# Kernel tuning notes

Measured on AMD Instinct MI355X. Metric: run time of the kernel, lower is better.

The kernel has to match this reference:

```python
import jax, jax.numpy as jnp
import numpy as np

B, L, D = 8, 2048, 1024
H = 16            # n_heads
E = 8             # num_experts
TOPK = 2
DH = D // H       # 64, per-head dim (== expert Linear dim)
CAP = TOPK * L // E  # 512 tokens per expert per batch (exact by construction)


def setup_inputs() -> dict:
    key = jax.random.key(0)
    ks = jax.random.split(key, 6)
    x = jax.random.normal(ks[0], (B, L, D), dtype=jnp.float32)
    gating_output = jax.nn.softmax(
        jax.random.normal(ks[1], (B, L, E), dtype=jnp.float32), axis=-1)
    # deterministic balanced routing: token l -> experts (l%E, (l+E//2)%E)
    l = jnp.arange(L)
    ind = jnp.stack([l % E, (l + E // 2) % E], axis=-1)  # [L,2]
    indices = jnp.broadcast_to(ind[None], (B, L, TOPK)).astype(jnp.int64)
    s = 1.0 / np.sqrt(DH)
    W1 = jax.random.normal(ks[2], (DH, DH), dtype=jnp.float32) * s
    b1 = jax.random.normal(ks[3], (DH,), dtype=jnp.float32) * 0.01
    W2 = jax.random.normal(ks[4], (DH, DH), dtype=jnp.float32) * s
    b2 = jax.random.normal(ks[5], (DH,), dtype=jnp.float32) * 0.01
    return {"x": x, "gating_output": gating_output, "indices": indices,
            "W1": W1, "b1": b1, "W2": W2, "b2": b2}


def _expert(xh, W1, b1, W2, b2):
    # xh: [B,H,C,d]. Shared expert (expert_fix) applied to gathered tokens.
    q = jnp.einsum('bhcd,ed->bhce', xh, W1) + b1
    k = jnp.einsum('bhcd,ed->bhce', xh, W2) + b2
    adj = jax.nn.gelu(jnp.einsum('bhid,bhjd->bhij', q, k), approximate=False)
    adj = jax.nn.softmax(adj, axis=-1)  # dropout: identity in eval
    out = jnp.einsum('bhij,bhjd->bhid', adj, xh)
    Bb, Hh, C, d = out.shape
    return out.transpose(0, 2, 1, 3).reshape(Bb, C, Hh * d)  # [B,C,D]


def reference(x, gating_output, indices, W1, b1, W2, b2):
    Bx, Lx, Dx = x.shape
    final = jnp.zeros_like(x)
    brow = jnp.arange(Bx)[:, None]  # [B,1]
    for i in range(E):
        mask = (indices == i).any(axis=-1)  # [B,L] bool, exactly CAP true/row
        idx = jax.vmap(lambda m: jnp.nonzero(m, size=CAP)[0])(mask)  # [B,C]
        xt = jnp.take_along_axis(x, idx[:, :, None], axis=1)  # [B,C,D]
        xh = xt.reshape(Bx, CAP, H, DH).transpose(0, 2, 1, 3)  # [B,H,C,d]
        out = _expert(xh, W1, b1, W2, b2)  # [B,C,D]
        g = jnp.take_along_axis(gating_output[..., i], idx, axis=1)  # [B,C]
        final = final.at[brow, idx].add(out * g[:, :, None])
    return final
```

## Files before the change

### kernel.cpp

```cpp
#include <hip/hip_runtime.h>
#include <hip/hip_bf16.h>
#include <cmath>


typedef _Float16 h16;
typedef __attribute__((ext_vector_type(4))) _Float16 half4;
typedef __attribute__((ext_vector_type(8))) _Float16 half8;
typedef __attribute__((ext_vector_type(4))) float f32x4;
typedef __attribute__((ext_vector_type(4))) unsigned int uint4v;

#define B_ 8
#define L_ 2048
#define D_ 1024
#define H_ 16
#define DH_ 64
#define L2E 1.4426950408f

#define XT_LD 520
#define XT_OFF 0
#define KW_OFF 66560
#define BETA_OFF 132096
#define AUX_OFF 134144
#define WC_OFF 134672
#define SMEM_BYTES 143888

__device__ __forceinline__ float gelu_fast(float v) {
  float e = __builtin_amdgcn_exp2f(v * fmaf(v * v, -0.10294357f, -2.3021957f));
  return v * __builtin_amdgcn_rcpf(1.f + e);
}

__global__ __launch_bounds__(512) void moe_prewc(
    const float* __restrict__ W1, const float* __restrict__ b1,
    const float* __restrict__ W2, const float* __restrict__ b2,
    float* __restrict__ ws)
{
  int bx = blockIdx.x;
  if (bx < 8) {
    int t = bx * 512 + threadIdx.x;
    int d = t >> 6, f = t & 63;
    float acc = 0.f;
    for (int e = 0; e < 64; ++e) acc += W2[e * 64 + f] * W1[e * 64 + d];
    ws[t] = acc;
  } else {
    int tid = threadIdx.x;
    if (tid < 64) {
      float acc = 0.f;
      for (int e = 0; e < 64; ++e) acc += b2[e] * W1[e * 64 + tid];
      ws[4096 + tid] = acc;
    } else if (tid < 128) {
      int f = tid - 64; float acc = 0.f;
      for (int e = 0; e < 64; ++e) acc += b1[e] * W2[e * 64 + f];
      ws[4160 + f] = acc;
    } else if (tid == 128) {
      float acc = 0.f;
      for (int e = 0; e < 64; ++e) acc += b1[e] * b2[e];
      ws[4224] = acc;
    }
  }
}

__global__ __launch_bounds__(1024) void moe_attn(
    const float* __restrict__ x, const float* __restrict__ gating,
    const float* __restrict__ wsc, float* __restrict__ out)
{
  extern __shared__ char smem[];
  h16*   XTh  = (h16*)(smem + XT_OFF);
  char*  KWb  = smem + KW_OFF;
  float* beta = (float*)(smem + BETA_OFF);
  float* bc   = (float*)(smem + AUX_OFF);
  float* wb   = bc + 64;
  float* bbp  = wb + 64;
  h16*   WCh  = (h16*)(smem + WC_OFF);

  const int tid  = threadIdx.x;
  const int wave = tid >> 6;
  const int lane = tid & 63;
  const int l15  = lane & 15;
  const int lg   = lane >> 4;
  const int bx   = blockIdx.x;
  const int h    = bx & 15;
  const int m    = (bx >> 4) & 3;
  const int b    = bx >> 6;

  for (int t = tid; t < 4096; t += 1024) {
    int c = t >> 3, dc = t & 7;
    int l = 8 * (c >> 1) + m + 4 * (c & 1);
    const float* gp = x + ((size_t)(b * L_ + l)) * D_ + h * DH_ + dc * 8;
    float vv[8];
    *(float4*)(vv)     = *(const float4*)(gp);
    *(float4*)(vv + 4) = *(const float4*)(gp + 4);
#pragma unroll
    for (int j = 0; j < 8; ++j)
      XTh[(dc * 8 + j) * XT_LD + c] = (h16)vv[j];
  }
  for (int t = tid; t < 4096; t += 1024)
    WCh[(t >> 6) * 72 + (t & 63)] = (h16)wsc[t];
  if (tid < 64) bc[tid] = wsc[4096 + tid];
  else if (tid < 128) wb[tid - 64] = wsc[4096 + tid];
  else if (tid == 128) *bbp = wsc[4224];
  __syncthreads();

  if (tid < 512) {
    int n = tid;
    float acc = *bbp;
    for (int f = 0; f < 64; ++f) acc += (float)XTh[f * XT_LD + n] * wb[f];
    beta[n] = acc;
  }
  for (int mt = wave; mt < 32; mt += 16) {
    int n0 = mt * 16;
    int tok = n0 + l15;
    half8 a0, a1;
#pragma unroll
    for (int j = 0; j < 8; ++j) {
      a0[j] = XTh[(lg * 8 + j) * XT_LD + tok];
      a1[j] = XTh[(32 + lg * 8 + j) * XT_LD + tok];
    }
#pragma unroll
    for (int ct = 0; ct < 4; ++ct) {
      const half8 bw0 = *(const half8*)(WCh + (ct * 16 + l15) * 72 + lg * 8);
      const half8 bw1 = *(const half8*)(WCh + (ct * 16 + l15) * 72 + 32 + lg * 8);
      f32x4 acc = {0.f, 0.f, 0.f, 0.f};
      acc = __builtin_amdgcn_mfma_f32_16x16x32_f16(a0, bw0, acc, 0, 0, 0);
      acc = __builtin_amdgcn_mfma_f32_16x16x32_f16(a1, bw1, acc, 0, 0, 0);
      int d = ct * 16 + l15;
      float bcd = bc[d];
#pragma unroll
      for (int r = 0; r < 4; ++r) {
        int row = n0 + lg * 4 + r;
        int byteoff = row * 128 + ((((d >> 3) ^ (row & 7)) << 4) | ((d & 7) << 1));
        *(h16*)(KWb + byteoff) = (h16)(acc[r] + bcd);
      }
    }
  }
  __syncthreads();

  const int g0 = (lg ^ (l15 & 7)) << 4;
  const int g1 = ((4 + lg) ^ (l15 & 7)) << 4;

  for (int qi = 0; qi < 2; ++qi) {
    const int m0 = (wave + qi * 16) * 16;
    const int qrow = m0 + l15;
    const int ql = 8 * (qrow >> 1) + m + 4 * (qrow & 1);
    const float* qp = x + ((size_t)(b * L_ + ql)) * D_ + h * DH_;

    half8 bq0, bq1;
    {
      const float4 A0 = *(const float4*)(qp + lg * 8);
      const float4 A1 = *(const float4*)(qp + lg * 8 + 4);
      const float4 B0 = *(const float4*)(qp + 32 + lg * 8);
      const float4 B1 = *(const float4*)(qp + 32 + lg * 8 + 4);
      bq0[0] = (h16)A0.x; bq0[1] = (h16)A0.y; bq0[2] = (h16)A0.z; bq0[3] = (h16)A0.w;
      bq0[4] = (h16)A1.x; bq0[5] = (h16)A1.y; bq0[6] = (h16)A1.z; bq0[7] = (h16)A1.w;
      bq1[0] = (h16)B0.x; bq1[1] = (h16)B0.y; bq1[2] = (h16)B0.z; bq1[3] = (h16)B0.w;
      bq1[4] = (h16)B1.x; bq1[5] = (h16)B1.y; bq1[6] = (h16)B1.z; bq1[7] = (h16)B1.w;
    }

    f32x4 o0 = {0.f,0.f,0.f,0.f}, o1 = o0, o2 = o0, o3 = o0;
    float Sl = 0.f, R = -1e30f, Ml2 = 0.f;

    for (int it = 0; it < 16; ++it) {
      f32x4 sa0, sa1;
      {
        int t = it * 2;
        f32x4 bv = *(const f32x4*)(beta + t * 16 + lg * 4);
        const char* kr = KWb + (t * 16 + l15) * 128;
        half8 ka0 = *(const half8*)(kr + g0);
        half8 ka1 = *(const half8*)(kr + g1);
        bv  = __builtin_amdgcn_mfma_f32_16x16x32_f16(ka0, bq0, bv, 0, 0, 0);
        sa0 = __builtin_amdgcn_mfma_f32_16x16x32_f16(ka1, bq1, bv, 0, 0, 0);
      }
      {
        int t = it * 2 + 1;
        f32x4 bv = *(const f32x4*)(beta + t * 16 + lg * 4);
        const char* kr = KWb + (t * 16 + l15) * 128;
        half8 ka0 = *(const half8*)(kr + g0);
        half8 ka1 = *(const half8*)(kr + g1);
        bv  = __builtin_amdgcn_mfma_f32_16x16x32_f16(ka0, bq0, bv, 0, 0, 0);
        sa1 = __builtin_amdgcn_mfma_f32_16x16x32_f16(ka1, bq1, bv, 0, 0, 0);
      }
      float cm = fmaxf(fmaxf(fmaxf(sa0[0], sa0[1]), fmaxf(sa0[2], sa0[3])),
                       fmaxf(fmaxf(sa1[0], sa1[1]), fmaxf(sa1[2], sa1[3])));
      cm = fmaxf(cm, __shfl_xor(cm, 16));
      cm = fmaxf(cm, __shfl_xor(cm, 32));
      bool tr = cm > R + 8.f;
      if (__any(tr)) {
        float Rn = tr ? cm : R;
        float Mn = fmaxf(gelu_fast(Rn), 0.f);
        float Ml2n = Mn * L2E;
        float scl = __builtin_amdgcn_exp2f(Ml2 - Ml2n);
        Sl *= scl; o0 *= scl; o1 *= scl; o2 *= scl; o3 *= scl;
        R = Rn; Ml2 = Ml2n;
      }
      float p00 = __builtin_amdgcn_exp2f(fmaf(gelu_fast(sa0[0]), L2E, -Ml2));
      float p01 = __builtin_amdgcn_exp2f(fmaf(gelu_fast(sa0[1]), L2E, -Ml2));
      float p02 = __builtin_amdgcn_exp2f(fmaf(gelu_fast(sa0[2]), L2E, -Ml2));
      float p03 = __builtin_amdgcn_exp2f(fmaf(gelu_fast(sa0[3]), L2E, -Ml2));
      float p10 = __builtin_amdgcn_exp2f(fmaf(gelu_fast(sa1[0]), L2E, -Ml2));
      float p11 = __builtin_amdgcn_exp2f(fmaf(gelu_fast(sa1[1]), L2E, -Ml2));
      float p12 = __builtin_amdgcn_exp2f(fmaf(gelu_fast(sa1[2]), L2E, -Ml2));
      float p13 = __builtin_amdgcn_exp2f(fmaf(gelu_fast(sa1[3]), L2E, -Ml2));
      Sl += ((p00 + p01) + (p02 + p03)) + ((p10 + p11) + (p12 + p13));
      uint4v pw;
      pw[0] = __builtin_bit_cast(unsigned int, __builtin_amdgcn_cvt_pkrtz(p00, p01));
      pw[1] = __builtin_bit_cast(unsigned int, __builtin_amdgcn_cvt_pkrtz(p02, p03));
      pw[2] = __builtin_bit_cast(unsigned int, __builtin_amdgcn_cvt_pkrtz(p10, p11));
      pw[3] = __builtin_bit_cast(unsigned int, __builtin_amdgcn_cvt_pkrtz(p12, p13));
      const half8 pB = __builtin_bit_cast(half8, pw);
      {
        const h16* ap = XTh + l15 * XT_LD + it * 32 + lg * 4;
#pragma unroll
        for (int ct = 0; ct < 4; ++ct) {
          const h16* app = ap + ct * 16 * XT_LD;
          const half4 lo = *(const half4*)(app);
          const half4 hi = *(const half4*)(app + 16);
          const half8 av = {lo[0], lo[1], lo[2], lo[3], hi[0], hi[1], hi[2], hi[3]};
          if      (ct == 0) o0 = __builtin_amdgcn_mfma_f32_16x16x32_f16(av, pB, o0, 0, 0, 0);
          else if (ct == 1) o1 = __builtin_amdgcn_mfma_f32_16x16x32_f16(av, pB, o1, 0, 0, 0);
          else if (ct == 2) o2 = __builtin_amdgcn_mfma_f32_16x16x32_f16(av, pB, o2, 0, 0, 0);
          else              o3 = __builtin_amdgcn_mfma_f32_16x16x32_f16(av, pB, o3, 0, 0, 0);
        }
      }
    }
    float Sv = Sl;
    Sv += __shfl_xor(Sv, 16);
    Sv += __shfl_xor(Sv, 32);
    const float* gp = gating + ((size_t)(b * L_ + ql)) * 8;
    float gv = gp[m] + gp[m + 4];
    float scale = gv * __builtin_amdgcn_rcpf(Sv);
    float* op = out + ((size_t)(b * L_ + ql)) * D_ + h * DH_ + lg * 4;
    *(f32x4*)(op)      = o0 * scale;
    *(f32x4*)(op + 16) = o1 * scale;
    *(f32x4*)(op + 32) = o2 * scale;
    *(f32x4*)(op + 48) = o3 * scale;
  }
}

extern "C" void kernel_launch(void* const* d_in, const int* in_sizes, int n_in,
                              void* d_out, int out_size, void* d_ws, size_t ws_size,
                              hipStream_t stream) {
  const float* x      = (const float*)d_in[0];
  const float* gating = (const float*)d_in[1];
  const float* W1 = (const float*)d_in[3];
  const float* b1 = (const float*)d_in[4];
  const float* W2 = (const float*)d_in[5];
  const float* b2 = (const float*)d_in[6];
  float* ws = (float*)d_ws;

  static bool attr_set = false;
  if (!attr_set) {
    hipFuncSetAttribute(reinterpret_cast<const void*>(moe_attn),
                        hipFuncAttributeMaxDynamicSharedMemorySize, SMEM_BYTES);
    attr_set = true;
  }
  moe_prewc<<<dim3(9), dim3(512), 0, stream>>>(W1, b1, W2, b2, ws);
  moe_attn<<<dim3(512), dim3(1024), SMEM_BYTES, stream>>>(
      x, gating, ws, (float*)d_out);
}
```

Before: 115.0 us.

## Process both query tiles per wave together to reuse K and X loads

The two sequential query-tile passes are fused into one loop, so each wave processes two 16-row query tiles at once. Each K fragment and X fragment read from shared memory then feeds two MFMAs. The XOR-swizzled K layout is replaced by a padded pitch of 136 bytes, and launch bounds now request waves-per-EU 4. The aim is to halve LDS traffic per MFMA and give the scheduler more independent MFMA work, at the cost of more registers for two accumulator sets and extra shared memory.

New measurement: 126.0 us. +9.6%, slower.

```diff
diff --git a/kernel.cpp b/kernel.cpp
--- a/kernel.cpp
+++ b/kernel.cpp
@@ -18,11 +18,12 @@
 
 #define XT_LD 520
 #define XT_OFF 0
+#define KW_PITCH 136
 #define KW_OFF 66560
-#define BETA_OFF 132096
-#define AUX_OFF 134144
-#define WC_OFF 134672
-#define SMEM_BYTES 143888
+#define BETA_OFF 136192
+#define AUX_OFF 138240
+#define WC_OFF 138768
+#define SMEM_BYTES 147984
 
 __device__ __forceinline__ float gelu_fast(float v) {
   float e = __builtin_amdgcn_exp2f(v * fmaf(v * v, -0.10294357f, -2.3021957f));
@@ -59,7 +60,7 @@
   }
 }
 
-__global__ __launch_bounds__(1024) void moe_attn(
+__global__ __launch_bounds__(1024, 4) void moe_attn(
     const float* __restrict__ x, const float* __restrict__ gating,
     const float* __restrict__ wsc, float* __restrict__ out)
 {
@@ -127,111 +128,181 @@
 #pragma unroll
       for (int r = 0; r < 4; ++r) {
         int row = n0 + lg * 4 + r;
-        int byteoff = row * 128 + ((((d >> 3) ^ (row & 7)) << 4) | ((d & 7) << 1));
-        *(h16*)(KWb + byteoff) = (h16)(acc[r] + bcd);
+        *(h16*)(KWb + row * KW_PITCH + d * 2) = (h16)(acc[r] + bcd);
       }
     }
   }
   __syncthreads();
 
-  const int g0 = (lg ^ (l15 & 7)) << 4;
-  const int g1 = ((4 + lg) ^ (l15 & 7)) << 4;
-
-  for (int qi = 0; qi < 2; ++qi) {
-    const int m0 = (wave + qi * 16) * 16;
-    const int qrow = m0 + l15;
-    const int ql = 8 * (qrow >> 1) + m + 4 * (qrow & 1);
-    const float* qp = x + ((size_t)(b * L_ + ql)) * D_ + h * DH_;
-
-    half8 bq0, bq1;
+  const int g0 = lg * 16;
+  const int g1 = 64 + lg * 16;
+
+  const int m0a = wave * 16;
+  const int m0b = (wave + 16) * 16;
+  const int qra = m0a + l15, qrb = m0b + l15;
+  const int qla = 8 * (qra >> 1) + m + 4 * (qra & 1);
+  const int qlb = 8 * (qrb >> 1) + m + 4 * (qrb & 1);
+  const float* qpa = x + ((size_t)(b * L_ + qla)) * D_ + h * DH_;
+  const float* qpb = x + ((size_t)(b * L_ + qlb)) * D_ + h * DH_;
+
+  half8 bqa0, bqa1, bqb0, bqb1;
+  {
+    const float4 A0 = *(const float4*)(qpa + lg * 8);
+    const float4 A1 = *(const float4*)(qpa + lg * 8 + 4);
+    const float4 A2 = *(const float4*)(qpa + 32 + lg * 8);
+    const float4 A3 = *(const float4*)(qpa + 32 + lg * 8 + 4);
+    bqa0[0]=(h16)A0.x; bqa0[1]=(h16)A0.y; bqa0[2]=(h16)A0.z; bqa0[3]=(h16)A0.w;
+    bqa0[4]=(h16)A1.x; bqa0[5]=(h16)A1.y; bqa0[6]=(h16)A1.z; bqa0[7]=(h16)A1.w;
+    bqa1[0]=(h16)A2.x; bqa1[1]=(h16)A2.y; bqa1[2]=(h16)A2.z; bqa1[3]=(h16)A2.w;
+    bqa1[4]=(h16)A3.x; bqa1[5]=(h16)A3.y; bqa1[6]=(h16)A3.z; bqa1[7]=(h16)A3.w;
+    const float4 B0 = *(const float4*)(qpb + lg * 8);
+    const float4 B1 = *(const float4*)(qpb + lg * 8 + 4);
+    const float4 B2 = *(const float4*)(qpb + 32 + lg * 8);
+    const float4 B3 = *(const float4*)(qpb + 32 + lg * 8 + 4);
+    bqb0[0]=(h16)B0.x; bqb0[1]=(h16)B0.y; bqb0[2]=(h16)B0.z; bqb0[3]=(h16)B0.w;
+    bqb0[4]=(h16)B1.x; bqb0[5]=(h16)B1.y; bqb0[6]=(h16)B1.z; bqb0[7]=(h16)B1.w;
+    bqb1[0]=(h16)B2.x; bqb1[1]=(h16)B2.y; bqb1[2]=(h16)B2.z; bqb1[3]=(h16)B2.w;
+    bqb1[4]=(h16)B3.x; bqb1[5]=(h16)B3.y; bqb1[6]=(h16)B3.z; bqb1[7]=(h16)B3.w;
+  }
+
+  f32x4 oa0 = {0.f,0.f,0.f,0.f}, oa1 = oa0, oa2 = oa0, oa3 = oa0;
+  f32x4 ob0 = oa0, ob1 = oa0, ob2 = oa0, ob3 = oa0;
+  float Sla = 0.f, Ra = -1e30f, Mla = 0.f;
+  float Slb = 0.f, Rb = -1e30f, Mlb = 0.f;
+
+  for (int it = 0; it < 16; ++it) {
+    const int t0 = it * 2, t1 = it * 2 + 1;
+    const char* kr0 = KWb + (t0 * 16 + l15) * KW_PITCH;
+    const char* kr1 = KWb + (t1 * 16 + l15) * KW_PITCH;
+    const half8 ka00 = *(const half8*)(kr0 + g0);
+    const half8 ka01 = *(const half8*)(kr0 + g1);
+    const half8 ka10 = *(const half8*)(kr1 + g0);
+    const half8 ka11 = *(const half8*)(kr1 + g1);
+    const f32x4 bv0 = *(const f32x4*)(beta + t0 * 16 + lg * 4);
+    const f32x4 bv1 = *(const f32x4*)(beta + t1 * 16 + lg * 4);
+
+    f32x4 s0a = __builtin_amdgcn_mfma_f32_16x16x32_f16(ka00, bqa0, bv0, 0, 0, 0);
+    s0a = __builtin_amdgcn_mfma_f32_16x16x32_f16(ka01, bqa1, s0a, 0, 0, 0);
+    f32x4 s1a = __builtin_amdgcn_mfma_f32_16x16x32_f16(ka10, bqa0, bv1, 0, 0, 0);
+    s1a = __builtin_amdgcn_mfma_f32_16x16x32_f16(ka11, bqa1, s1a, 0, 0, 0);
+    f32x4 s0b = __builtin_amdgcn_mfma_f32_16x16x32_f16(ka00, bqb0, bv0, 0, 0, 0);
+    s0b = __builtin_amdgcn_mfma_f32_16x16x32_f16(ka01, bqb1, s0b, 0, 0, 0);
+    f32x4 s1b = __builtin_amdgcn_mfma_f32_16x16x32_f16(ka10, bqb0, bv1, 0, 0, 0);
+    s1b = __builtin_amdgcn_mfma_f32_16x16x32_f16(ka11, bqb1, s1b, 0, 0, 0);
+
+    float cma = fmaxf(fmaxf(fmaxf(s0a[0], s0a[1]), fmaxf(s0a[2], s0a[3])),
+                      fmaxf(fmaxf(s1a[0], s1a[1]), fmaxf(s1a[2], s1a[3])));
+    float cmb = fmaxf(fmaxf(fmaxf(s0b[0], s0b[1]), fmaxf(s0b[2], s0b[3])),
+                      fmaxf(fmaxf(s1b[0], s1b[1]), fmaxf(s1b[2], s1b[3])));
+    cma = fmaxf(cma, __shfl_xor(cma, 16));
+    cma = fmaxf(cma, __shfl_xor(cma, 32));
+    cmb = fmaxf(cmb, __shfl_xor(cmb, 16));
+    cmb = fmaxf(cmb, __shfl_xor(cmb, 32));
+    bool tra = cma > Ra + 8.f;
+    bool trb = cmb > Rb + 8.f;
+    if (__any(tra || trb)) {
+      float Rna = tra ? cma : Ra;
+      float Mna = fmaxf(gelu_fast(Rna), 0.f) * L2E;
+      float sca = __builtin_amdgcn_exp2f(Mla - Mna);
+      Sla *= sca; oa0 *= sca; oa1 *= sca; oa2 *= sca; oa3 *= sca;
+      Ra = Rna; Mla = Mna;
+      float Rnb = trb ? cmb : Rb;
+      float Mnb = fmaxf(gelu_fast(Rnb), 0.f) * L2E;
+      float scb = __builtin_amdgcn_exp2f(Mlb - Mnb);
+      Slb *= scb; ob0 *= scb; ob1 *= scb; ob2 *= scb; ob3 *= scb;
+      Rb = Rnb; Mlb = Mnb;
+    }
+    float pa0 = __builtin_amdgcn_exp2f(fmaf(gelu_fast(s0a[0]), L2E, -Mla));
+    float pa1 = __builtin_amdgcn_exp2f(fmaf(gelu_fast(s0a[1]), L2E, -Mla));
+    float pa2 = __builtin_amdgcn_exp2f(fmaf(gelu_fast(s0a[2]), L2E, -Mla));
+    float pa3 = __builtin_amdgcn_exp2f(fmaf(gelu_fast(s0a[3]), L2E, -Mla));
+    float pa4 = __builtin_amdgcn_exp2f(fmaf(gelu_fast(s1a[0]), L2E, -Mla));
+    float pa5 = __builtin_amdgcn_exp2f(fmaf(gelu_fast(s1a[1]), L2E, -Mla));
+    float pa6 = __builtin_amdgcn_exp2f(fmaf(gelu_fast(s1a[2]), L2E, -Mla));
+    float pa7 = __builtin_amdgcn_exp2f(fmaf(gelu_fast(s1a[3]), L2E, -Mla));
+    Sla += ((pa0 + pa1) + (pa2 + pa3)) + ((pa4 + pa5) + (pa6 + pa7));
+    uint4v pwa;
+    pwa[0] = __builtin_bit_cast(unsigned int, __builtin_amdgcn_cvt_pkrtz(pa0, pa1));
+    pwa[1] = __builtin_bit_cast(unsigned int, __builtin_amdgcn_cvt_pkrtz(pa2, pa3));
+    pwa[2] = __builtin_bit_cast(unsigned int, __builtin_amdgcn_cvt_pkrtz(pa4, pa5));
+    pwa[3] = __builtin_bit_cast(unsigned int, __builtin_amdgcn_cvt_pkrtz(pa6, pa7));
+    const half8 pBa = __builtin_bit_cast(half8, pwa);
+
+    float pb0 = __builtin_amdgcn_exp2f(fmaf(gelu_fast(s0b[0]), L2E, -Mlb));
+    float pb1 = __builtin_amdgcn_exp2f(fmaf(gelu_fast(s0b[1]), L2E, -Mlb));
+    float pb2 = __builtin_amdgcn_exp2f(fmaf(gelu_fast(s0b[2]), L2E, -Mlb));
+    float pb3 = __builtin_amdgcn_exp2f(fmaf(gelu_fast(s0b[3]), L2E, -Mlb));
+    float pb4 = __builtin_amdgcn_exp2f(fmaf(gelu_fast(s1b[0]), L2E, -Mlb));
+    float pb5 = __builtin_amdgcn_exp2f(fmaf(gelu_fast(s1b[1]), L2E, -Mlb));
+    float pb6 = __builtin_amdgcn_exp2f(fmaf(gelu_fast(s1b[2]), L2E, -Mlb));
+    float pb7 = __builtin_amdgcn_exp2f(fmaf(gelu_fast(s1b[3]), L2E, -Mlb));
+    Slb += ((pb0 + pb1) + (pb2 + pb3)) + ((pb4 + pb5) + (pb6 + pb7));
+    uint4v pwb;
+    pwb[0] = __builtin_bit_cast(unsigned int, __builtin_amdgcn_cvt_pkrtz(pb0, pb1));
+    pwb[1] = __builtin_bit_cast(unsigned int, __builtin_amdgcn_cvt_pkrtz(pb2, pb3));
+    pwb[2] = __builtin_bit_cast(unsigned int, __builtin_amdgcn_cvt_pkrtz(pb4, pb5));
+    pwb[3] = __builtin_bit_cast(unsigned int, __builtin_amdgcn_cvt_pkrtz(pb6, pb7));
+    const half8 pBb = __builtin_bit_cast(half8, pwb);
+
+    const h16* ap = XTh + l15 * XT_LD + it * 32 + lg * 4;
     {
-      const float4 A0 = *(const float4*)(qp + lg * 8);
-      const float4 A1 = *(const float4*)(qp + lg * 8 + 4);
-      const float4 B0 = *(const float4*)(qp + 32 + lg * 8);
-      const float4 B1 = *(const float4*)(qp + 32 + lg * 8 + 4);
-      bq0[0] = (h16)A0.x; bq0[1] = (h16)A0.y; bq0[2] = (h16)A0.z; bq0[3] = (h16)A0.w;
-      bq0[4] = (h16)A1.x; bq0[5] = (h16)A1.y; bq0[6] = (h16)A1.z; bq0[7] = (h16)A1.w;
-      bq1[0] = (h16)B0.x; bq1[1] = (h16)B0.y; bq1[2] = (h16)B0.z; bq1[3] = (h16)B0.w;
-      bq1[4] = (h16)B1.x; bq1[5] = (h16)B1.y; bq1[6] = (h16)B1.z; bq1[7] = (h16)B1.w;
-    }
-
-    f32x4 o0 = {0.f,0.f,0.f,0.f}, o1 = o0, o2 = o0, o3 = o0;
-    float Sl = 0.f, R = -1e30f, Ml2 = 0.f;
-
-    for (int it = 0; it < 16; ++it) {
-      f32x4 sa0, sa1;
-      {
-        int t = it * 2;
-        f32x4 bv = *(const f32x4*)(beta + t * 16 + lg * 4);
-        const char* kr = KWb + (t * 16 + l15) * 128;
-        half8 ka0 = *(const half8*)(kr + g0);
-        half8 ka1 = *(const half8*)(kr + g1);
-        bv  = __builtin_amdgcn_mfma_f32_16x16x32_f16(ka0, bq0, bv, 0, 0, 0);
-        sa0 = __builtin_amdgcn_mfma_f32_16x16x32_f16(ka1, bq1, bv, 0, 0, 0);
-      }
-      {
-        int t = it * 2 + 1;
-        f32x4 bv = *(const f32x4*)(beta + t * 16 + lg * 4);
-        const char* kr = KWb + (t * 16 + l15) * 128;
-        half8 ka0 = *(const half8*)(kr + g0);
-        half8 ka1 = *(const half8*)(kr + g1);
-        bv  = __builtin_amdgcn_mfma_f32_16x16x32_f16(ka0, bq0, bv, 0, 0, 0);
-        sa1 = __builtin_amdgcn_mfma_f32_16x16x32_f16(ka1, bq1, bv, 0, 0, 0);
-      }
-      float cm = fmaxf(fmaxf(fmaxf(sa0[0], sa0[1]), fmaxf(sa0[2], sa0[3])),
-                       fmaxf(fmaxf(sa1[0], sa1[1]), fmaxf(sa1[2], sa1[3])));
-      cm = fmaxf(cm, __shfl_xor(cm, 16));
-      cm = fmaxf(cm, __shfl_xor(cm, 32));
-      bool tr = cm > R + 8.f;
-      if (__any(tr)) {
-        float Rn = tr ? cm : R;
-        float Mn = fmaxf(gelu_fast(Rn), 0.f);
-        float Ml2n = Mn * L2E;
-        float scl = __builtin_amdgcn_exp2f(Ml2 - Ml2n);
-        Sl *= scl; o0 *= scl; o1 *= scl; o2 *= scl; o3 *= scl;
-        R = Rn; Ml2 = Ml2n;
-      }
-      float p00 = __builtin_amdgcn_exp2f(fmaf(gelu_fast(sa0[0]), L2E, -Ml2));
-      float p01 = __builtin_amdgcn_exp2f(fmaf(gelu_fast(sa0[1]), L2E, -Ml2));
-      float p02 = __builtin_amdgcn_exp2f(fmaf(gelu_fast(sa0[2]), L2E, -Ml2));
-      float p03 = __builtin_amdgcn_exp2f(fmaf(gelu_fast(sa0[3]), L2E, -Ml2));
-      float p10 = __builtin_amdgcn_exp2f(fmaf(gelu_fast(sa1[0]), L2E, -Ml2));
-      float p11 = __builtin_amdgcn_exp2f(fmaf(gelu_fast(sa1[1]), L2E, -Ml2));
-      float p12 = __builtin_amdgcn_exp2f(fmaf(gelu_fast(sa1[2]), L2E, -Ml2));
-      float p13 = __builtin_amdgcn_exp2f(fmaf(gelu_fast(sa1[3]), L2E, -Ml2));
-      Sl += ((p00 + p01) + (p02 + p03)) + ((p10 + p11) + (p12 + p13));
-      uint4v pw;
-      pw[0] = __builtin_bit_cast(unsigned int, __builtin_amdgcn_cvt_pkrtz(p00, p01));
-      pw[1] = __builtin_bit_cast(unsigned int, __builtin_amdgcn_cvt_pkrtz(p02, p03));
-      pw[2] = __builtin_bit_cast(unsigned int, __builtin_amdgcn_cvt_pkrtz(p10, p11));
-      pw[3] = __builtin_bit_cast(unsigned int, __builtin_amdgcn_cvt_pkrtz(p12, p13));
-      const half8 pB = __builtin_bit_cast(half8, pw);
-      {
-        const h16* ap = XTh + l15 * XT_LD + it * 32 + lg * 4;
-#pragma unroll
-        for (int ct = 0; ct < 4; ++ct) {
-          const h16* app = ap + ct * 16 * XT_LD;
-          const half4 lo = *(const half4*)(app);
-          const half4 hi = *(const half4*)(app + 16);
-          const half8 av = {lo[0], lo[1], lo[2], lo[3], hi[0], hi[1], hi[2], hi[3]};
-          if      (ct == 0) o0 = __builtin_amdgcn_mfma_f32_16x16x32_f16(av, pB, o0, 0, 0, 0);
-          else if (ct == 1) o1 = __builtin_amdgcn_mfma_f32_16x16x32_f16(av, pB, o1, 0, 0, 0);
-          else if (ct == 2) o2 = __builtin_amdgcn_mfma_f32_16x16x32_f16(av, pB, o2, 0, 0, 0);
-          else              o3 = __builtin_amdgcn_mfma_f32_16x16x32_f16(av, pB, o3, 0, 0, 0);
-        }
-      }
-    }
-    float Sv = Sl;
+      const half4 lo = *(const half4*)(ap);
+      const half4 hi = *(const half4*)(ap + 16);
+      const half8 av = {lo[0],lo[1],lo[2],lo[3],hi[0],hi[1],hi[2],hi[3]};
+      oa0 = __builtin_amdgcn_mfma_f32_16x16x32_f16(av, pBa, oa0, 0, 0, 0);
+      ob0 = __builtin_amdgcn_mfma_f32_16x16x32_f16(av, pBb, ob0, 0, 0, 0);
+    }
+    {
+      const h16* app = ap + 16 * XT_LD;
+      const half4 lo = *(const half4*)(app);
+      const half4 hi = *(const half4*)(app + 16);
+      const half8 av = {lo[0],lo[1],lo[2],lo[3],hi[0],hi[1],hi[2],hi[3]};
+      oa1 = __builtin_amdgcn_mfma_f32_16x16x32_f16(av, pBa, oa1, 0, 0, 0);
+      ob1 = __builtin_amdgcn_mfma_f32_16x16x32_f16(av, pBb, ob1, 0, 0, 0);
+    }
+    {
+      const h16* app = ap + 32 * XT_LD;
+      const half4 lo = *(const half4*)(app);
+      const half4 hi = *(const half4*)(app + 16);
+      const half8 av = {lo[0],lo[1],lo[2],lo[3],hi[0],hi[1],hi[2],hi[3]};
+      oa2 = __builtin_amdgcn_mfma_f32_16x16x32_f16(av, pBa, oa2, 0, 0, 0);
+      ob2 = __builtin_amdgcn_mfma_f32_16x16x32_f16(av, pBb, ob2, 0, 0, 0);
+    }
+    {
+      const h16* app = ap + 48 * XT_LD;
+      const half4 lo = *(const half4*)(app);
+      const half4 hi = *(const half4*)(app + 16);
+      const half8 av = {lo[0],lo[1],lo[2],lo[3],hi[0],hi[1],hi[2],hi[3]};
+      oa3 = __builtin_amdgcn_mfma_f32_16x16x32_f16(av, pBa, oa3, 0, 0, 0);
+      ob3 = __builtin_amdgcn_mfma_f32_16x16x32_f16(av, pBb, ob3, 0, 0, 0);
+    }
+  }
+
+  {
+    float Sv = Sla;
     Sv += __shfl_xor(Sv, 16);
     Sv += __shfl_xor(Sv, 32);
-    const float* gp = gating + ((size_t)(b * L_ + ql)) * 8;
+    const float* gp = gating + ((size_t)(b * L_ + qla)) * 8;
     float gv = gp[m] + gp[m + 4];
     float scale = gv * __builtin_amdgcn_rcpf(Sv);
-    float* op = out + ((size_t)(b * L_ + ql)) * D_ + h * DH_ + lg * 4;
-    *(f32x4*)(op)      = o0 * scale;
-    *(f32x4*)(op + 16) = o1 * scale;
-    *(f32x4*)(op + 32) = o2 * scale;
-    *(f32x4*)(op + 48) = o3 * scale;
+    float* op = out + ((size_t)(b * L_ + qla)) * D_ + h * DH_ + lg * 4;
+    *(f32x4*)(op)      = oa0 * scale;
+    *(f32x4*)(op + 16) = oa1 * scale;
+    *(f32x4*)(op + 32) = oa2 * scale;
+    *(f32x4*)(op + 48) = oa3 * scale;
+  }
+  {
+    float Sv = Slb;
+    Sv += __shfl_xor(Sv, 16);
+    Sv += __shfl_xor(Sv, 32);
+    const float* gp = gating + ((size_t)(b * L_ + qlb)) * 8;
+    float gv = gp[m] + gp[m + 4];
+    float scale = gv * __builtin_amdgcn_rcpf(Sv);
+    float* op = out + ((size_t)(b * L_ + qlb)) * D_ + h * DH_ + lg * 4;
+    *(f32x4*)(op)      = ob0 * scale;
+    *(f32x4*)(op + 16) = ob1 * scale;
+    *(f32x4*)(op + 32) = ob2 * scale;
+    *(f32x4*)(op + 48) = ob3 * scale;
   }
 }
 
```
